# Kernel optimization log

Hardware: AMD Instinct MI355X
Metric: run time of the kernel (lower is better)

The kernel has to match this reference:

```python
import jax, jax.numpy as jnp
import numpy as np

D_MODEL = 512
NH_ATTN = 8
D_STATE = 64
HEADDIM = 128
D_INNER = 2 * D_MODEL          # 1024
NHEADS = D_INNER // HEADDIM    # 8
CONV_K = 4
CONV_DIM = D_INNER + 2 * D_STATE            # 1152
D_IN_PROJ = 2 * D_INNER + 2 * D_STATE + NHEADS  # 2184
B, S, M = 2, 2048, 1024
EPS = 1e-5


def setup_inputs() -> dict:
    key = jax.random.key(0)
    ks = jax.random.split(key, 10)
    s = 0.02
    return {
        'x': jax.random.normal(ks[0], (B, S, D_MODEL), dtype=jnp.float32),
        'memory': jax.random.normal(ks[1], (B, M, D_MODEL), dtype=jnp.float32),
        'pad_mask': jnp.ones((B, S, 1), dtype=jnp.float32),
        'ln1_g': jnp.ones((D_MODEL,)), 'ln1_b': jnp.zeros((D_MODEL,)),
        'ln2_g': jnp.ones((D_MODEL,)), 'ln2_b': jnp.zeros((D_MODEL,)),
        'W_in': jax.random.normal(ks[2], (D_IN_PROJ, D_MODEL)) * s,
        'conv_w': jax.random.normal(ks[3], (CONV_DIM, 1, CONV_K)) * s,
        'conv_b': jnp.zeros((CONV_DIM,)),
        'dt_bias': jnp.log(jnp.expm1(jax.random.uniform(ks[4], (NHEADS,), minval=0.001, maxval=0.1))),
        'A_log': jnp.log(jnp.arange(1, NHEADS + 1, dtype=jnp.float32)),
        'D_skip': jnp.ones((NHEADS,)),
        'rms_w': jnp.ones((D_INNER,)),
        'W_out': jax.random.normal(ks[5], (D_MODEL, D_INNER)) * s,
        'Wqkv': jax.random.normal(ks[6], (3 * D_MODEL, D_MODEL)) * s,
        'bqkv': jnp.zeros((3 * D_MODEL,)),
        'Wo': jax.random.normal(ks[7], (D_MODEL, D_MODEL)) * s,
        'bo': jnp.zeros((D_MODEL,)),
    }


def _layernorm(x, g, b):
    m = jnp.mean(x, axis=-1, keepdims=True)
    v = jnp.mean((x - m) ** 2, axis=-1, keepdims=True)
    return (x - m) * jax.lax.rsqrt(v + EPS) * g + b


def _mamba(x, W_in, conv_w, conv_b, dt_bias, A_log, D_skip, rms_w, W_out):
    b, s, _ = x.shape
    zxbcdt = x @ W_in.T                                     # [b,s,2184]
    z, xBC, dt = jnp.split(zxbcdt, [D_INNER, D_INNER + CONV_DIM], axis=-1)
    # causal depthwise conv over time on (x, B, C)
    xt = jnp.transpose(xBC, (0, 2, 1))                      # [b,C,s]
    xt = jax.lax.conv_general_dilated(
        xt, conv_w, (1,), [(CONV_K - 1, 0)],
        feature_group_count=CONV_DIM,
        dimension_numbers=('NCH', 'OIH', 'NCH'))
    xBC = jax.nn.silu(jnp.transpose(xt, (0, 2, 1)) + conv_b)
    xs, Bm, Cm = jnp.split(xBC, [D_INNER, D_INNER + D_STATE], axis=-1)
    dt = jax.nn.softplus(dt + dt_bias)                      # [b,s,H]
    A = -jnp.exp(A_log)                                     # [H]
    xh = xs.reshape(b, s, NHEADS, HEADDIM)                  # [b,s,H,P]

    def step(h, inps):
        dt_t, B_t, C_t, x_t = inps                          # [b,H],[b,N],[b,N],[b,H,P]
        decay = jnp.exp(dt_t * A)                           # [b,H]
        h = h * decay[..., None, None] + (dt_t[..., None, None] * x_t[..., None]) * B_t[:, None, None, :]
        y = jnp.einsum('bhpn,bn->bhp', h, C_t)
        return h, y

    h0 = jnp.zeros((b, NHEADS, HEADDIM, D_STATE), dtype=x.dtype)
    _, ys = jax.lax.scan(step, h0, (dt.transpose(1, 0, 2), Bm.transpose(1, 0, 2),
                                    Cm.transpose(1, 0, 2), xh.transpose(1, 0, 2, 3)))
    y = ys.transpose(1, 0, 2, 3) + D_skip[None, None, :, None] * xh
    y = y.reshape(b, s, D_INNER) * jax.nn.silu(z)           # gated
    y = y * jax.lax.rsqrt(jnp.mean(y * y, axis=-1, keepdims=True) + EPS) * rms_w
    return y @ W_out.T


def _cross_attn(q_in, memory, Wqkv, bqkv, Wo, bo):
    b, s, _ = q_in.shape
    m = memory.shape[1]
    dh = D_MODEL // NH_ATTN
    q = (q_in @ Wqkv[:D_MODEL].T + bqkv[:D_MODEL]).reshape(b, s, NH_ATTN, dh)
    k = (memory @ Wqkv[D_MODEL:2 * D_MODEL].T + bqkv[D_MODEL:2 * D_MODEL]).reshape(b, m, NH_ATTN, dh)
    v = (memory @ Wqkv[2 * D_MODEL:].T + bqkv[2 * D_MODEL:]).reshape(b, m, NH_ATTN, dh)
    scores = jnp.einsum('bqhd,bkhd->bhqk', q, k) / jnp.sqrt(jnp.asarray(dh, q.dtype))
    p = jax.nn.softmax(scores, axis=-1)
    out = jnp.einsum('bhqk,bkhd->bqhd', p, v).reshape(b, s, D_MODEL)
    return out @ Wo.T + bo


def reference(x, memory, pad_mask, ln1_g, ln1_b, ln2_g, ln2_b, W_in, conv_w, conv_b,
              dt_bias, A_log, D_skip, rms_w, W_out, Wqkv, bqkv, Wo, bo):
    residual = x
    xn = _layernorm(x, ln1_g, ln1_b) * pad_mask
    x = residual + _mamba(xn, W_in, conv_w, conv_b, dt_bias, A_log, D_skip, rms_w, W_out)
    h = _layernorm(x, ln2_g, ln2_b)
    x = x + _cross_attn(h, memory, Wqkv, bqkv, Wo, bo)
    return x
```

## Files before the change

### kernel.cpp

```cpp
#include <hip/hip_runtime.h>
#include <hip/hip_bf16.h>

typedef __hip_bfloat16 bf16;
typedef short v8s __attribute__((ext_vector_type(8)));
typedef short v4s __attribute__((ext_vector_type(4)));
typedef float v4f __attribute__((ext_vector_type(4)));

__device__ __forceinline__ void gll16(const bf16* g, bf16* l) {
    __builtin_amdgcn_global_load_lds(
        (const __attribute__((address_space(1))) unsigned int*)g,
        (__attribute__((address_space(3))) unsigned int*)l, 16, 0, 0);
}
__device__ __forceinline__ float bf2f(short s) {
    return __uint_as_float(((unsigned int)(unsigned short)s) << 16);
}

__global__ __launch_bounds__(256) void pre_kernel(
    const float* __restrict__ x, const float* __restrict__ g,
    const float* __restrict__ bt, const float* __restrict__ mask,
    bf16* __restrict__ xn,
    const float* __restrict__ W_in, const float* __restrict__ W_out,
    const float* __restrict__ Wqkv, const float* __restrict__ Wo,
    const float* __restrict__ mem,
    bf16* __restrict__ Winb, bf16* __restrict__ Woutb, bf16* __restrict__ Wqkvb,
    bf16* __restrict__ Wob, bf16* __restrict__ memb)
{
    int tid = threadIdx.x;
    if (blockIdx.x < 4096) {
        int row = blockIdx.x;
        const float* xr = x + (size_t)row * 512;
        float v0 = xr[tid], v1 = xr[tid + 256];
        float s = v0 + v1, ss = v0 * v0 + v1 * v1;
        #pragma unroll
        for (int o = 32; o; o >>= 1) { s += __shfl_xor(s, o); ss += __shfl_xor(ss, o); }
        __shared__ float l1[4], l2[4];
        if ((tid & 63) == 0) { l1[tid >> 6] = s; l2[tid >> 6] = ss; }
        __syncthreads();
        s = l1[0] + l1[1] + l1[2] + l1[3];
        ss = l2[0] + l2[1] + l2[2] + l2[3];
        float mean = s * (1.f / 512.f);
        float var = ss * (1.f / 512.f) - mean * mean;
        float rs = rsqrtf(var + 1e-5f);
        float mk = mask[row];
        xn[(size_t)row * 512 + tid] =
            __float2bfloat16(((v0 - mean) * rs * g[tid] + bt[tid]) * mk);
        xn[(size_t)row * 512 + tid + 256] =
            __float2bfloat16(((v1 - mean) * rs * g[tid + 256] + bt[tid + 256]) * mk);
        return;
    }
    int i = (blockIdx.x - 4096) * 256 + tid;
    const int E0 = 2184 * 512;
    const int E1 = E0 + 524288;
    const int E2 = E1 + 786432;
    const int E3 = E2 + 262144;
    const int E4 = E3 + 1048576;
    if (i < E0) {
        Winb[i] = __float2bfloat16(W_in[i]);
    } else if (i < E1) {
        int j = i - E0; Woutb[j] = __float2bfloat16(W_out[j]);
    } else if (i < E2) {
        int j = i - E1; Wqkvb[j] = __float2bfloat16(Wqkv[j]);
    } else if (i < E3) {
        int j = i - E2; Wob[j] = __float2bfloat16(Wo[j]);
    } else if (i < E4) {
        int j = i - E3; memb[j] = __float2bfloat16(mem[j]);
    }
}

__global__ __launch_bounds__(256) void ln_kernel(
    const float* __restrict__ x, const float* __restrict__ g,
    const float* __restrict__ bt, bf16* __restrict__ out)
{
    int row = blockIdx.x, tid = threadIdx.x;
    const float* xr = x + (size_t)row * 512;
    float v0 = xr[tid], v1 = xr[tid + 256];
    float s = v0 + v1, ss = v0 * v0 + v1 * v1;
    #pragma unroll
    for (int o = 32; o; o >>= 1) { s += __shfl_xor(s, o); ss += __shfl_xor(ss, o); }
    __shared__ float l1[4], l2[4];
    if ((tid & 63) == 0) { l1[tid >> 6] = s; l2[tid >> 6] = ss; }
    __syncthreads();
    s = l1[0] + l1[1] + l1[2] + l1[3];
    ss = l2[0] + l2[1] + l2[2] + l2[3];
    float mean = s * (1.f / 512.f);
    float var = ss * (1.f / 512.f) - mean * mean;
    float rs = rsqrtf(var + 1e-5f);
    out[(size_t)row * 512 + tid] =
        __float2bfloat16((v0 - mean) * rs * g[tid] + bt[tid]);
    out[(size_t)row * 512 + tid + 256] =
        __float2bfloat16((v1 - mean) * rs * g[tid + 256] + bt[tid + 256]);
}

__global__ __launch_bounds__(256) void gemm_bt(
    const bf16* __restrict__ Aall, const bf16* __restrict__ Wall,
    const float* __restrict__ bias, const float* __restrict__ resid,
    void* __restrict__ Cout,
    int M, int N, int K, int ldA, int ldW, int ldC,
    long sA1, long sA2, long sW1, long sW2, long sC1, long sC2,
    int zdiv, int outbf16)
{
    __shared__ bf16 lA[2][128 * 32];
    __shared__ bf16 lB[2][128 * 32];
    int z = blockIdx.z;
    int zb = z / zdiv, zh = z - zb * zdiv;
    const bf16* A = Aall + zb * sA1 + zh * sA2;
    const bf16* W = Wall + zb * sW1 + zh * sW2;
    long coff = zb * sC1 + zh * sC2;

    int bm = blockIdx.x * 128, bn = blockIdx.y * 128;
    int tid = threadIdx.x, lane = tid & 63, wv = tid >> 6;
    int wr = (wv >> 1) * 64, wc = (wv & 1) * 64;
    int lr15 = lane & 15, lk8 = (lane >> 4) * 8;

    v4f acc[4][4] = {};
    int sr = tid >> 2, sc = (tid & 3) * 8;
    const bf16* Abase = A + (size_t)(bm + sr) * ldA + sc;
    const bf16* Wbase = W + (size_t)(bn + sr) * ldW + sc;

    int nt = K >> 5, cur = 0;
    gll16(Abase, &lA[0][tid * 8]);
    gll16(Abase + (size_t)64 * ldA, &lA[0][tid * 8 + 2048]);
    gll16(Wbase, &lB[0][tid * 8]);
    gll16(Wbase + (size_t)64 * ldW, &lB[0][tid * 8 + 2048]);
    __syncthreads();
    for (int t = 0; t < nt; ++t) {
        if (t + 1 < nt) {
            int k0 = (t + 1) * 32;
            gll16(Abase + k0, &lA[cur ^ 1][tid * 8]);
            gll16(Abase + (size_t)64 * ldA + k0, &lA[cur ^ 1][tid * 8 + 2048]);
            gll16(Wbase + k0, &lB[cur ^ 1][tid * 8]);
            gll16(Wbase + (size_t)64 * ldW + k0, &lB[cur ^ 1][tid * 8 + 2048]);
        }
        v8s af[4], bfr[4];
        #pragma unroll
        for (int i = 0; i < 4; ++i)
            af[i] = *(const v8s*)&lA[cur][(wr + i * 16 + lr15) * 32 + lk8];
        #pragma unroll
        for (int i = 0; i < 4; ++i)
            bfr[i] = *(const v8s*)&lB[cur][(wc + i * 16 + lr15) * 32 + lk8];
        #pragma unroll
        for (int mi = 0; mi < 4; ++mi)
            #pragma unroll
            for (int ni = 0; ni < 4; ++ni)
                acc[mi][ni] = __builtin_amdgcn_mfma_f32_16x16x32_bf16(
                    af[mi], bfr[ni], acc[mi][ni], 0, 0, 0);
        __syncthreads();
        cur ^= 1;
    }
    int r0 = bm + wr + (lane >> 4) * 4;
    int c0 = bn + wc + lr15;
    #pragma unroll
    for (int mi = 0; mi < 4; ++mi) {
        #pragma unroll
        for (int ni = 0; ni < 4; ++ni) {
            int col = c0 + ni * 16;
            if (col < N) {
                float bv = bias ? bias[col] : 0.f;
                #pragma unroll
                for (int r = 0; r < 4; ++r) {
                    int row = r0 + mi * 16 + r;
                    long idx = coff + (long)row * ldC + col;
                    float v = acc[mi][ni][r] + bv;
                    if (resid) v += resid[idx];
                    if (outbf16) ((bf16*)Cout)[idx] = __float2bfloat16(v);
                    else ((float*)Cout)[idx] = v;
                }
            }
        }
    }
}

__global__ __launch_bounds__(256) void gemm64(
    const bf16* __restrict__ Aall, const bf16* __restrict__ Wall,
    const float* __restrict__ bias, const float* __restrict__ resid,
    void* __restrict__ Cout,
    int M, int N, int K, int ldA, int ldW, int ldC,
    long sA1, long sA2, long sW1, long sW2, long sC1, long sC2,
    int zdiv, int outbf16)
{
    __shared__ bf16 lA[2][64 * 32];
    __shared__ bf16 lB[2][64 * 32];
    int z = blockIdx.z;
    int zb = z / zdiv, zh = z - zb * zdiv;
    const bf16* A = Aall + zb * sA1 + zh * sA2;
    const bf16* W = Wall + zb * sW1 + zh * sW2;
    long coff = zb * sC1 + zh * sC2;

    int bm = blockIdx.x * 64, bn = blockIdx.y * 64;
    int tid = threadIdx.x, lane = tid & 63, wv = tid >> 6;
    int wr = (wv >> 1) * 32, wc = (wv & 1) * 32;
    int lr15 = lane & 15, lk8 = (lane >> 4) * 8;

    v4f acc[2][2] = {};
    int sr = tid >> 2, sc = (tid & 3) * 8;
    const bf16* Abase = A + (size_t)(bm + sr) * ldA + sc;
    const bf16* Wbase = W + (size_t)(bn + sr) * ldW + sc;

    int nt = K >> 5, cur = 0;
    gll16(Abase, &lA[0][tid * 8]);
    gll16(Wbase, &lB[0][tid * 8]);
    __syncthreads();
    for (int t = 0; t < nt; ++t) {
        if (t + 1 < nt) {
            int k0 = (t + 1) * 32;
            gll16(Abase + k0, &lA[cur ^ 1][tid * 8]);
            gll16(Wbase + k0, &lB[cur ^ 1][tid * 8]);
        }
        v8s a0 = *(const v8s*)&lA[cur][(wr + lr15) * 32 + lk8];
        v8s a1 = *(const v8s*)&lA[cur][(wr + 16 + lr15) * 32 + lk8];
        v8s b0 = *(const v8s*)&lB[cur][(wc + lr15) * 32 + lk8];
        v8s b1 = *(const v8s*)&lB[cur][(wc + 16 + lr15) * 32 + lk8];
        acc[0][0] = __builtin_amdgcn_mfma_f32_16x16x32_bf16(a0, b0, acc[0][0], 0, 0, 0);
        acc[0][1] = __builtin_amdgcn_mfma_f32_16x16x32_bf16(a0, b1, acc[0][1], 0, 0, 0);
        acc[1][0] = __builtin_amdgcn_mfma_f32_16x16x32_bf16(a1, b0, acc[1][0], 0, 0, 0);
        acc[1][1] = __builtin_amdgcn_mfma_f32_16x16x32_bf16(a1, b1, acc[1][1], 0, 0, 0);
        __syncthreads();
        cur ^= 1;
    }
    int r0 = bm + wr + (lane >> 4) * 4;
    int c0 = bn + wc + lr15;
    #pragma unroll
    for (int mi = 0; mi < 2; ++mi) {
        #pragma unroll
        for (int ni = 0; ni < 2; ++ni) {
            int col = c0 + ni * 16;
            if (col < N) {
                float bv = bias ? bias[col] : 0.f;
                #pragma unroll
                for (int r = 0; r < 4; ++r) {
                    int row = r0 + mi * 16 + r;
                    long idx = coff + (long)row * ldC + col;
                    float v = acc[mi][ni][r] + bv;
                    if (resid) v += resid[idx];
                    if (outbf16) ((bf16*)Cout)[idx] = __float2bfloat16(v);
                    else ((float*)Cout)[idx] = v;
                }
            }
        }
    }
}

__global__ __launch_bounds__(256) void flash_attn(
    const bf16* __restrict__ qb, const bf16* __restrict__ kvb,
    const bf16* __restrict__ vT, bf16* __restrict__ attn)
{
    __shared__ bf16 lK[2][128 * 64];
    __shared__ bf16 lV[2][64 * 128];
    __shared__ bf16 lP[4][16 * 128];
    int z = blockIdx.z;
    int b = z >> 3, h = z & 7;
    int q0 = blockIdx.x * 64;
    int tid = threadIdx.x, lane = tid & 63, wv = tid >> 6;
    int l15 = lane & 15, l4 = lane >> 4, l7 = lane & 7;

    const bf16* Qg = qb + (size_t)(b * 2048 + q0) * 512 + h * 64;
    const bf16* Kg = kvb + (size_t)b * 1024 * 1024 + h * 64;
    const bf16* Vg = vT + (size_t)z * 64 * 1024;

    v8s af[2];
    #pragma unroll
    for (int ks = 0; ks < 2; ++ks)
        af[ks] = *(const v8s*)(Qg + (size_t)(wv * 16 + l15) * 512 + (ks * 4 + l4) * 8);

    #pragma unroll
    for (int pass = 0; pass < 4; ++pass) {
        int s = pass * 256 + tid;
        int kr = s >> 3, kc = s & 7;
        gll16(Kg + (size_t)kr * 1024 + ((kc ^ (kr & 7)) << 3), &lK[0][s * 8]);
        int vr = s >> 4, vc = s & 15;
        int vsw = (vc & 8) | ((vc & 7) ^ (vr & 7));
        gll16(Vg + (size_t)vr * 1024 + (vsw << 3), &lV[0][s * 8]);
    }
    __syncthreads();

    v4f o[4] = {};
    v4f m_run = (v4f){-1e30f, -1e30f, -1e30f, -1e30f};
    v4f l_run = (v4f){0.f, 0.f, 0.f, 0.f};
    bf16* lPw = &lP[wv][0];

    int cur = 0;
    #pragma unroll 1
    for (int t = 0; t < 8; ++t) {
        if (t + 1 < 8) {
            int k0n = (t + 1) * 128;
            #pragma unroll
            for (int pass = 0; pass < 4; ++pass) {
                int s = pass * 256 + tid;
                int kr = s >> 3, kc = s & 7;
                gll16(Kg + (size_t)(k0n + kr) * 1024 + ((kc ^ (kr & 7)) << 3),
                      &lK[cur ^ 1][s * 8]);
                int vr = s >> 4, vc = s & 15;
                int vsw = (vc & 8) | ((vc & 7) ^ (vr & 7));
                gll16(Vg + (size_t)vr * 1024 + k0n + (vsw << 3), &lV[cur ^ 1][s * 8]);
            }
        }
        v4f s_acc[8];
        #pragma unroll
        for (int kn = 0; kn < 8; ++kn) {
            s_acc[kn] = (v4f){0.f, 0.f, 0.f, 0.f};
            #pragma unroll
            for (int ks = 0; ks < 2; ++ks) {
                v8s kv = *(const v8s*)&lK[cur][(kn * 16 + l15) * 64 +
                                               (((ks * 4 + l4) ^ l7) << 3)];
                s_acc[kn] = __builtin_amdgcn_mfma_f32_16x16x32_bf16(
                    af[ks], kv, s_acc[kn], 0, 0, 0);
            }
        }
        v4f tm;
        #pragma unroll
        for (int r = 0; r < 4; ++r) {
            float m0 = fmaxf(fmaxf(s_acc[0][r], s_acc[1][r]),
                             fmaxf(s_acc[2][r], s_acc[3][r]));
            float m1 = fmaxf(fmaxf(s_acc[4][r], s_acc[5][r]),
                             fmaxf(s_acc[6][r], s_acc[7][r]));
            tm[r] = fmaxf(m0, m1);
        }
        #pragma unroll
        for (int off = 8; off >= 1; off >>= 1)
            #pragma unroll
            for (int r = 0; r < 4; ++r)
                tm[r] = fmaxf(tm[r], __shfl_xor(tm[r], off));
        v4f mnew, alpha;
        #pragma unroll
        for (int r = 0; r < 4; ++r) {
            mnew[r] = fmaxf(m_run[r], 0.125f * tm[r]);
            alpha[r] = __expf(m_run[r] - mnew[r]);
        }
        m_run = mnew;
        v4f rs = {0.f, 0.f, 0.f, 0.f};
        #pragma unroll
        for (int kn = 0; kn < 8; ++kn)
            #pragma unroll
            for (int r = 0; r < 4; ++r) {
                float pv = __expf(0.125f * s_acc[kn][r] - mnew[r]);
                s_acc[kn][r] = pv;
                rs[r] += pv;
            }
        #pragma unroll
        for (int off = 8; off >= 1; off >>= 1)
            #pragma unroll
            for (int r = 0; r < 4; ++r)
                rs[r] += __shfl_xor(rs[r], off);
        #pragma unroll
        for (int r = 0; r < 4; ++r)
            l_run[r] = l_run[r] * alpha[r] + rs[r];
        #pragma unroll
        for (int ni = 0; ni < 4; ++ni)
            #pragma unroll
            for (int r = 0; r < 4; ++r)
                o[ni][r] *= alpha[r];
        #pragma unroll
        for (int kn = 0; kn < 8; ++kn)
            #pragma unroll
            for (int r = 0; r < 4; ++r) {
                int row = l4 * 4 + r;
                int col = kn * 16 + l15;
                int c = col >> 3;
                int csw = (c & 8) | ((c & 7) ^ (row & 7));
                lPw[row * 128 + (csw << 3) + (col & 7)] =
                    __float2bfloat16(s_acc[kn][r]);
            }
        #pragma unroll
        for (int ni = 0; ni < 4; ++ni)
            #pragma unroll
            for (int ks = 0; ks < 4; ++ks) {
                int ck = ks * 4 + l4;
                int psw = (ck & 8) | ((ck & 7) ^ l7);
                v8s pv = *(const v8s*)&lPw[l15 * 128 + (psw << 3)];
                v8s vv = *(const v8s*)&lV[cur][(ni * 16 + l15) * 128 + (psw << 3)];
                o[ni] = __builtin_amdgcn_mfma_f32_16x16x32_bf16(
                    pv, vv, o[ni], 0, 0, 0);
            }
        __syncthreads();
        cur ^= 1;
    }
    v4f inv;
    #pragma unroll
    for (int r = 0; r < 4; ++r) inv[r] = 1.f / l_run[r];
    #pragma unroll
    for (int ni = 0; ni < 4; ++ni)
        #pragma unroll
        for (int r = 0; r < 4; ++r) {
            int row = q0 + wv * 16 + l4 * 4 + r;
            int col = h * 64 + ni * 16 + l15;
            attn[(size_t)(b * 2048 + row) * 512 + col] =
                __float2bfloat16(o[ni][r] * inv[r]);
        }
}

__global__ __launch_bounds__(256) void conv_dt(
    const bf16* __restrict__ zx, const float* __restrict__ cw,
    const float* __restrict__ cb, bf16* __restrict__ out,
    const float* __restrict__ dt_bias, const float* __restrict__ A_log,
    float* __restrict__ dtb, float* __restrict__ decb)
{
    int tid = threadIdx.x;
    if (blockIdx.x >= 576) {
        int i = (blockIdx.x - 576) * 256 + tid;
        if (i >= 32768) return;
        int h = i & 7, row = i >> 3;
        float d = bf2f(((const short*)zx)[(size_t)row * 2184 + 2176 + h]) + dt_bias[h];
        float sp = d > 20.f ? d : log1pf(expf(d));
        dtb[i] = sp;
        decb[i] = expf(-expf(A_log[h]) * sp);
        return;
    }
    int idx = blockIdx.x * 256 + tid;
    int c4 = (idx % 288) * 4;
    int tb = (idx / 288) % 256;
    int b  = idx / (288 * 256);
    int t0 = tb * 8;
    const bf16* base = zx + (size_t)b * 2048 * 2184 + 1024 + c4;
    bf16* ob = out + ((size_t)(b * 2048 + t0)) * 1152 + c4;

    float wt[4][4];
    #pragma unroll
    for (int k = 0; k < 4; ++k)
        #pragma unroll
        for (int j = 0; j < 4; ++j) wt[j][k] = cw[(c4 + k) * 4 + j];
    v4f bias = *(const v4f*)(cb + c4);

    v4f r[11];
    #pragma unroll
    for (int j = 0; j < 11; ++j) {
        int ts = t0 - 3 + j;
        if (ts >= 0) {
            v4s raw = *(const v4s*)(base + (size_t)ts * 2184);
            #pragma unroll
            for (int k = 0; k < 4; ++k) r[j][k] = bf2f(raw[k]);
        } else r[j] = (v4f){0.f, 0.f, 0.f, 0.f};
    }
    #pragma unroll
    for (int t = 0; t < 8; ++t) {
        v4f acc = bias;
        #pragma unroll
        for (int k = 0; k < 4; ++k)
            acc[k] += wt[0][k] * r[t][k] + wt[1][k] * r[t + 1][k]
                    + wt[2][k] * r[t + 2][k] + wt[3][k] * r[t + 3][k];
        v4s res;
        #pragma unroll
        for (int k = 0; k < 4; ++k) {
            float v = acc[k] / (1.f + expf(-acc[k]));
            res[k] = (short)__bfloat16_as_ushort(__float2bfloat16(v));
        }
        *(v4s*)(ob + (size_t)t * 1152) = res;
    }
}

__global__ __launch_bounds__(256) void scan_p1(
    const bf16* __restrict__ conv, const float* __restrict__ dtb,
    const float* __restrict__ decb, const float* __restrict__ A_log,
    bf16* __restrict__ slocal, float* __restrict__ cdec)
{
    int chunk = blockIdx.x, bh = blockIdx.y;
    int b = bh >> 3, h = bh & 7;
    int tid = threadIdx.x;
    int wv = tid >> 6, lane = tid & 63;
    int nh = lane >> 5, psub = lane & 31;
    int p = wv * 32 + psub;
    __shared__ float lx[32][128];
    __shared__ float lB[32][64];
    __shared__ float ldt[32], ldec[32];
    const bf16* cb_ = conv + (size_t)b * 2048 * 1152;
    int t0 = chunk * 32;
    #pragma unroll
    for (int pass = 0; pass < 2; ++pass) {
        int s = pass * 256 + tid;
        int row = s >> 4, c8 = (s & 15) * 8;
        v8s raw = *(const v8s*)(cb_ + (size_t)(t0 + row) * 1152 + h * 128 + c8);
        v4f lo, hi;
        #pragma unroll
        for (int j = 0; j < 4; ++j) { lo[j] = bf2f(raw[j]); hi[j] = bf2f(raw[j + 4]); }
        *(v4f*)&lx[row][c8] = lo;
        *(v4f*)&lx[row][c8 + 4] = hi;
    }
    {
        int s = tid;
        int row = s >> 3, c8 = (s & 7) * 8;
        v8s raw = *(const v8s*)(cb_ + (size_t)(t0 + row) * 1152 + 1024 + c8);
        v4f lo, hi;
        #pragma unroll
        for (int j = 0; j < 4; ++j) { lo[j] = bf2f(raw[j]); hi[j] = bf2f(raw[j + 4]); }
        *(v4f*)&lB[row][c8] = lo;
        *(v4f*)&lB[row][c8 + 4] = hi;
    }
    if (tid < 32) {
        int ri = (b * 2048 + t0 + tid) * 8 + h;
        ldt[tid] = dtb[ri]; ldec[tid] = decb[ri];
    }
    __syncthreads();
    v4f hs[8] = {};
    float sdt = 0.f;
    #pragma unroll 2
    for (int t = 0; t < 32; ++t) {
        float dtv = ldt[t], dec = ldec[t];
        float c1 = dtv * lx[t][p];
        const v4f* Bp = (const v4f*)&lB[t][nh * 32];
        #pragma unroll
        for (int i = 0; i < 8; ++i) hs[i] = hs[i] * dec + Bp[i] * c1;
        sdt += dtv;
    }
    if (tid == 0) cdec[bh * 64 + chunk] = expf(-expf(A_log[h]) * sdt);
    bf16* S = slocal + ((size_t)bh * 64 + chunk) * 8192;
    #pragma unroll
    for (int i = 0; i < 8; ++i)
        #pragma unroll
        for (int j = 0; j < 4; ++j)
            S[(nh * 32 + i * 4 + j) * 128 + p] = __float2bfloat16(hs[i][j]);
}

__global__ __launch_bounds__(256) void scan_comb(
    const bf16* __restrict__ slocal, const float* __restrict__ cdec,
    bf16* __restrict__ hinit)
{
    int e = blockIdx.x * 256 + threadIdx.x;
    int bh = e >> 13, np = e & 8191;
    size_t base = (size_t)bh * 524288 + np;
    const float* cd = cdec + bh * 64;
    float hi = 0.f;
    for (int c = 0; c < 64; ++c) {
        size_t idx = base + (size_t)c * 8192;
        hinit[idx] = __float2bfloat16(hi);
        hi = hi * cd[c] + __bfloat162float(slocal[idx]);
    }
}

__global__ __launch_bounds__(256) void scan_p3(
    const bf16* __restrict__ conv, const float* __restrict__ dtb,
    const float* __restrict__ decb, const bf16* __restrict__ hinit,
    const float* __restrict__ Dskip, bf16* __restrict__ ybuf)
{
    int chunk = blockIdx.x, bh = blockIdx.y;
    int b = bh >> 3, h = bh & 7;
    int tid = threadIdx.x;
    int wv = tid >> 6, lane = tid & 63;
    int nh = lane >> 5, psub = lane & 31;
    int p = wv * 32 + psub;
    __shared__ float lx[32][128];
    __shared__ float lB[32][64];
    __shared__ float lC[32][64];
    __shared__ float ldt[32], ldec[32];
    const bf16* cb_ = conv + (size_t)b * 2048 * 1152;
    int t0 = chunk * 32;
    #pragma unroll
    for (int pass = 0; pass < 2; ++pass) {
        int s = pass * 256 + tid;
        int row = s >> 4, c8 = (s & 15) * 8;
        v8s raw = *(const v8s*)(cb_ + (size_t)(t0 + row) * 1152 + h * 128 + c8);
        v4f lo, hi;
        #pragma unroll
        for (int j = 0; j < 4; ++j) { lo[j] = bf2f(raw[j]); hi[j] = bf2f(raw[j + 4]); }
        *(v4f*)&lx[row][c8] = lo;
        *(v4f*)&lx[row][c8 + 4] = hi;
    }
    {
        int s = tid;
        int row = s >> 3, c8 = (s & 7) * 8;
        v8s rawB = *(const v8s*)(cb_ + (size_t)(t0 + row) * 1152 + 1024 + c8);
        v8s rawC = *(const v8s*)(cb_ + (size_t)(t0 + row) * 1152 + 1088 + c8);
        v4f lo, hi;
        #pragma unroll
        for (int j = 0; j < 4; ++j) { lo[j] = bf2f(rawB[j]); hi[j] = bf2f(rawB[j + 4]); }
        *(v4f*)&lB[row][c8] = lo;
        *(v4f*)&lB[row][c8 + 4] = hi;
        #pragma unroll
        for (int j = 0; j < 4; ++j) { lo[j] = bf2f(rawC[j]); hi[j] = bf2f(rawC[j + 4]); }
        *(v4f*)&lC[row][c8] = lo;
        *(v4f*)&lC[row][c8 + 4] = hi;
    }
    if (tid < 32) {
        int ri = (b * 2048 + t0 + tid) * 8 + h;
        ldt[tid] = dtb[ri]; ldec[tid] = decb[ri];
    }
    __syncthreads();
    v4f hs[8];
    const bf16* H = hinit + ((size_t)bh * 64 + chunk) * 8192;
    #pragma unroll
    for (int i = 0; i < 8; ++i)
        #pragma unroll
        for (int j = 0; j < 4; ++j)
            hs[i][j] = __bfloat162float(H[(nh * 32 + i * 4 + j) * 128 + p]);
    float Dk = Dskip[h];
    #pragma unroll 2
    for (int t = 0; t < 32; ++t) {
        float dtv = ldt[t], dec = ldec[t];
        float xv = lx[t][p];
        float c1 = dtv * xv;
        const v4f* Bp = (const v4f*)&lB[t][nh * 32];
        const v4f* Cp = (const v4f*)&lC[t][nh * 32];
        v4f ya = {0.f, 0.f, 0.f, 0.f};
        #pragma unroll
        for (int i = 0; i < 8; ++i) {
            hs[i] = hs[i] * dec + Bp[i] * c1;
            ya += hs[i] * Cp[i];
        }
        float part = ya[0] + ya[1] + ya[2] + ya[3];
        part += __shfl_xor(part, 32);
        if (nh == 0)
            ybuf[((size_t)(b * 2048 + t0 + t)) * 1024 + h * 128 + p] =
                __float2bfloat16(part + Dk * xv);
    }
}

__global__ __launch_bounds__(256) void gate_rms(
    const bf16* __restrict__ ybuf, const bf16* __restrict__ zx,
    const float* __restrict__ rms_w, bf16* __restrict__ out)
{
    int row = blockIdx.x, tid = threadIdx.x;
    int i0 = tid * 4;
    v4s yv = *(const v4s*)(ybuf + (size_t)row * 1024 + i0);
    v4s zv = *(const v4s*)(zx + (size_t)row * 2184 + i0);
    v4f rw = *(const v4f*)(rms_w + i0);
    float vals[4];
    float ss = 0.f;
    #pragma unroll
    for (int j = 0; j < 4; ++j) {
        float y = bf2f(yv[j]);
        float z = bf2f(zv[j]);
        float g = y * (z / (1.f + expf(-z)));
        vals[j] = g;
        ss += g * g;
    }
    #pragma unroll
    for (int o = 32; o; o >>= 1) ss += __shfl_xor(ss, o);
    __shared__ float l[4];
    if ((tid & 63) == 0) l[tid >> 6] = ss;
    __syncthreads();
    ss = l[0] + l[1] + l[2] + l[3];
    float rs = rsqrtf(ss * (1.f / 1024.f) + 1e-5f);
    v4s o4;
    #pragma unroll
    for (int j = 0; j < 4; ++j)
        o4[j] = (short)__bfloat16_as_ushort(__float2bfloat16(vals[j] * rs * rw[j]));
    *(v4s*)(out + (size_t)row * 1024 + i0) = o4;
}

__global__ __launch_bounds__(256) void v_transpose(const bf16* __restrict__ kvb,
                                                   bf16* __restrict__ vT) {
    __shared__ bf16 t[64][68];
    int bh = blockIdx.y, b = bh >> 3, h = bh & 7;
    int m0 = blockIdx.x * 64;
    int tid = threadIdx.x;
    #pragma unroll
    for (int pass = 0; pass < 2; ++pass) {
        int s = pass * 256 + tid;
        int row = s >> 3, c8 = (s & 7) * 8;
        v8s v = *(const v8s*)(kvb + ((size_t)(b * 1024 + m0 + row)) * 1024 + 512 +
                              h * 64 + c8);
        *(v8s*)&t[row][c8] = v;
    }
    __syncthreads();
    #pragma unroll
    for (int pass = 0; pass < 2; ++pass) {
        int s = pass * 256 + tid;
        int d = s >> 3, m8 = (s & 7) * 8;
        bf16 tmp[8];
        #pragma unroll
        for (int j = 0; j < 8; ++j) tmp[j] = t[m8 + j][d];
        *(v8s*)(vT + ((size_t)(bh * 64 + d)) * 1024 + m0 + m8) = *(v8s*)&tmp[0];
    }
}

extern "C" void kernel_launch(void* const* d_in, const int* in_sizes, int n_in,
                              void* d_out, int out_size, void* d_ws, size_t ws_size,
                              hipStream_t stream) {
    (void)in_sizes; (void)n_in; (void)out_size; (void)ws_size;
    const float* x       = (const float*)d_in[0];
    const float* memory  = (const float*)d_in[1];
    const float* mask    = (const float*)d_in[2];
    const float* ln1_g   = (const float*)d_in[3];
    const float* ln1_b   = (const float*)d_in[4];
    const float* ln2_g   = (const float*)d_in[5];
    const float* ln2_b   = (const float*)d_in[6];
    const float* W_in    = (const float*)d_in[7];
    const float* conv_w  = (const float*)d_in[8];
    const float* conv_b  = (const float*)d_in[9];
    const float* dt_bias = (const float*)d_in[10];
    const float* A_log   = (const float*)d_in[11];
    const float* D_skip  = (const float*)d_in[12];
    const float* rms_w   = (const float*)d_in[13];
    const float* W_out   = (const float*)d_in[14];
    const float* Wqkv    = (const float*)d_in[15];
    const float* bqkv    = (const float*)d_in[16];
    const float* Wo      = (const float*)d_in[17];
    const float* bo      = (const float*)d_in[18];
    float* out = (float*)d_out;

    char* w = (char*)d_ws;
    bf16*  xn     = (bf16*)(w + 0);
    bf16*  Winb   = (bf16*)(w + 4194304);
    bf16*  Woutb  = (bf16*)(w + 6430720);
    bf16*  Wqkvb  = (bf16*)(w + 7479296);
    bf16*  Wob    = (bf16*)(w + 9052160);
    bf16*  memb   = (bf16*)(w + 9576448);
    bf16*  zx     = (bf16*)(w + 11673600);
    bf16*  conv   = (bf16*)(w + 47456256);
    float* dtb    = (float*)(w + 66330624);
    float* decb   = (float*)(w + 66461696);
    bf16*  ybuf   = (bf16*)(w + 66592768);
    bf16*  slocal = (bf16*)(w + 83369984);
    bf16*  hinit  = (bf16*)(w + 100147200);
    bf16*  ybf    = (bf16*)(w + 83369984);
    float* x2     = (float*)(w + 100147200);
    bf16*  hb     = (bf16*)(w + 108535808);
    bf16*  qb     = (bf16*)(w + 112730112);
    float* cdec   = (float*)(w + 116924416);
    bf16*  kvb    = (bf16*)(w + 116928512);
    bf16*  vT     = (bf16*)(w + 121122816);
    bf16*  attn   = (bf16*)(w + 123219968);
    bf16*  gout   = (bf16*)(w + 75497472);
    gout = (bf16*)(w + 29564928);
    (void)ybf;

    pre_kernel<<<18704, 256, 0, stream>>>(x, ln1_g, ln1_b, mask, xn,
                                          W_in, W_out, Wqkv, Wo, memory,
                                          Winb, Woutb, Wqkvb, Wob, memb);

    gemm_bt<<<dim3(32, 18, 1), 256, 0, stream>>>(
        xn, Winb, nullptr, nullptr, (void*)zx,
        4096, 2184, 512, 512, 512, 2184,
        0, 0, 0, 0, 0, 0, 1, 1);

    conv_dt<<<704, 256, 0, stream>>>(zx, conv_w, conv_b, conv,
                                     dt_bias, A_log, dtb, decb);

    scan_p1<<<dim3(64, 16), 256, 0, stream>>>(conv, dtb, decb, A_log, slocal, cdec);
    scan_comb<<<512, 256, 0, stream>>>(slocal, cdec, hinit);
    scan_p3<<<dim3(64, 16), 256, 0, stream>>>(conv, dtb, decb, hinit, D_skip, ybuf);

    gate_rms<<<4096, 256, 0, stream>>>(ybuf, zx, rms_w, gout);

    gemm64<<<dim3(64, 8, 1), 256, 0, stream>>>(
        gout, Woutb, nullptr, x, (void*)x2,
        4096, 512, 1024, 1024, 1024, 512,
        0, 0, 0, 0, 0, 0, 1, 0);

    ln_kernel<<<4096, 256, 0, stream>>>(x2, ln2_g, ln2_b, hb);

    gemm64<<<dim3(64, 8, 1), 256, 0, stream>>>(
        hb, Wqkvb, bqkv, nullptr, (void*)qb,
        4096, 512, 512, 512, 512, 512, 0, 0, 0, 0, 0, 0, 1, 1);
    gemm64<<<dim3(32, 16, 1), 256, 0, stream>>>(
        memb, Wqkvb + 512 * 512, bqkv + 512, nullptr, (void*)kvb,
        2048, 1024, 512, 512, 512, 1024, 0, 0, 0, 0, 0, 0, 1, 1);

    v_transpose<<<dim3(16, 16), 256, 0, stream>>>(kvb, vT);

    flash_attn<<<dim3(32, 1, 16), 256, 0, stream>>>(qb, kvb, vT, attn);

    gemm64<<<dim3(64, 8, 1), 256, 0, stream>>>(
        attn, Wob, bo, x2, (void*)out,
        4096, 512, 512, 512, 512, 512,
        0, 0, 0, 0, 0, 0, 1, 0);
}
```

Baseline: 196.3 us.

## Fuse causal conv and dt softplus into scan kernels; fuse V transpose into KV GEMM

Removes the standalone conv_dt kernel. Both scan_p1 and scan_p3 now load raw zx rows, with a 3-row halo, into LDS and compute the depthwise conv, SiLU, softplus(dt) and the decay inline. This drops the intermediate conv/dt/decay buffers and one launch, at the cost of computing the conv twice, once in each scan pass. The V transpose kernel is also removed: the KV projection GEMM epilogue now writes the transposed V directly as packed 4-element stores.

```diff
diff --git a/kernel.cpp b/kernel.cpp
--- a/kernel.cpp
+++ b/kernel.cpp
@@ -13,6 +13,9 @@
 }
 __device__ __forceinline__ float bf2f(short s) {
     return __uint_as_float(((unsigned int)(unsigned short)s) << 16);
+}
+__device__ __forceinline__ short f2bfs(float f) {
+    return (short)__bfloat16_as_ushort(__float2bfloat16(f));
 }
 
 __global__ __launch_bounds__(256) void pre_kernel(
@@ -176,7 +179,7 @@
     void* __restrict__ Cout,
     int M, int N, int K, int ldA, int ldW, int ldC,
     long sA1, long sA2, long sW1, long sW2, long sC1, long sC2,
-    int zdiv, int outbf16)
+    int zdiv, int outbf16, bf16* __restrict__ vTout)
 {
     __shared__ bf16 lA[2][64 * 32];
     __shared__ bf16 lB[2][64 * 32];
@@ -226,14 +229,26 @@
             int col = c0 + ni * 16;
             if (col < N) {
                 float bv = bias ? bias[col] : 0.f;
+                float vals[4];
                 #pragma unroll
                 for (int r = 0; r < 4; ++r) {
                     int row = r0 + mi * 16 + r;
                     long idx = coff + (long)row * ldC + col;
                     float v = acc[mi][ni][r] + bv;
                     if (resid) v += resid[idx];
+                    vals[r] = v;
                     if (outbf16) ((bf16*)Cout)[idx] = __float2bfloat16(v);
                     else ((float*)Cout)[idx] = v;
+                }
+                if (vTout && col >= 512) {
+                    int d = col - 512;
+                    int row0 = r0 + mi * 16;
+                    int bb = row0 >> 10, m0 = row0 & 1023;
+                    v4s pk;
+                    #pragma unroll
+                    for (int r = 0; r < 4; ++r) pk[r] = f2bfs(vals[r]);
+                    *(v4s*)(vTout + (((size_t)(bb * 8 + (d >> 6)) * 64 + (d & 63))
+                                     * 1024 + m0)) = pk;
                 }
             }
         }
@@ -388,68 +403,10 @@
         }
 }
 
-__global__ __launch_bounds__(256) void conv_dt(
+__global__ __launch_bounds__(256) void scan_p1(
     const bf16* __restrict__ zx, const float* __restrict__ cw,
-    const float* __restrict__ cb, bf16* __restrict__ out,
-    const float* __restrict__ dt_bias, const float* __restrict__ A_log,
-    float* __restrict__ dtb, float* __restrict__ decb)
-{
-    int tid = threadIdx.x;
-    if (blockIdx.x >= 576) {
-        int i = (blockIdx.x - 576) * 256 + tid;
-        if (i >= 32768) return;
-        int h = i & 7, row = i >> 3;
-        float d = bf2f(((const short*)zx)[(size_t)row * 2184 + 2176 + h]) + dt_bias[h];
-        float sp = d > 20.f ? d : log1pf(expf(d));
-        dtb[i] = sp;
-        decb[i] = expf(-expf(A_log[h]) * sp);
-        return;
-    }
-    int idx = blockIdx.x * 256 + tid;
-    int c4 = (idx % 288) * 4;
-    int tb = (idx / 288) % 256;
-    int b  = idx / (288 * 256);
-    int t0 = tb * 8;
-    const bf16* base = zx + (size_t)b * 2048 * 2184 + 1024 + c4;
-    bf16* ob = out + ((size_t)(b * 2048 + t0)) * 1152 + c4;
-
-    float wt[4][4];
-    #pragma unroll
-    for (int k = 0; k < 4; ++k)
-        #pragma unroll
-        for (int j = 0; j < 4; ++j) wt[j][k] = cw[(c4 + k) * 4 + j];
-    v4f bias = *(const v4f*)(cb + c4);
-
-    v4f r[11];
-    #pragma unroll
-    for (int j = 0; j < 11; ++j) {
-        int ts = t0 - 3 + j;
-        if (ts >= 0) {
-            v4s raw = *(const v4s*)(base + (size_t)ts * 2184);
-            #pragma unroll
-            for (int k = 0; k < 4; ++k) r[j][k] = bf2f(raw[k]);
-        } else r[j] = (v4f){0.f, 0.f, 0.f, 0.f};
-    }
-    #pragma unroll
-    for (int t = 0; t < 8; ++t) {
-        v4f acc = bias;
-        #pragma unroll
-        for (int k = 0; k < 4; ++k)
-            acc[k] += wt[0][k] * r[t][k] + wt[1][k] * r[t + 1][k]
-                    + wt[2][k] * r[t + 2][k] + wt[3][k] * r[t + 3][k];
-        v4s res;
-        #pragma unroll
-        for (int k = 0; k < 4; ++k) {
-            float v = acc[k] / (1.f + expf(-acc[k]));
-            res[k] = (short)__bfloat16_as_ushort(__float2bfloat16(v));
-        }
-        *(v4s*)(ob + (size_t)t * 1152) = res;
-    }
-}
-
-__global__ __launch_bounds__(256) void scan_p1(
-    const bf16* __restrict__ conv, const float* __restrict__ dtb,
-    const float* __restrict__ decb, const float* __restrict__ A_log,
+    const float* __restrict__ cb, const float* __restrict__ dt_bias,
+    const float* __restrict__ A_log,
     bf16* __restrict__ slocal, float* __restrict__ cdec)
 {
     int chunk = blockIdx.x, bh = blockIdx.y;
@@ -458,35 +415,84 @@
     int wv = tid >> 6, lane = tid & 63;
     int nh = lane >> 5, psub = lane & 31;
     int p = wv * 32 + psub;
-    __shared__ float lx[32][128];
+    __shared__ bf16 rawx[35][136];
+    __shared__ bf16 rawB[35][72];
+    __shared__ bf16 lxb[32][128];
     __shared__ float lB[32][64];
+    __shared__ v4f lwx[128];
+    __shared__ v4f lwB[64];
+    __shared__ float lcb[192];
     __shared__ float ldt[32], ldec[32];
-    const bf16* cb_ = conv + (size_t)b * 2048 * 1152;
+    const bf16* zb_ = zx + (size_t)b * 2048 * 2184;
     int t0 = chunk * 32;
-    #pragma unroll
-    for (int pass = 0; pass < 2; ++pass) {
-        int s = pass * 256 + tid;
-        int row = s >> 4, c8 = (s & 15) * 8;
-        v8s raw = *(const v8s*)(cb_ + (size_t)(t0 + row) * 1152 + h * 128 + c8);
-        v4f lo, hi;
-        #pragma unroll
-        for (int j = 0; j < 4; ++j) { lo[j] = bf2f(raw[j]); hi[j] = bf2f(raw[j + 4]); }
-        *(v4f*)&lx[row][c8] = lo;
-        *(v4f*)&lx[row][c8 + 4] = hi;
-    }
+    for (int s = tid; s < 560; s += 256) {
+        int rr = s >> 4, c8 = (s & 15) * 8;
+        int zr = t0 - 3 + rr;
+        v8s v = {};
+        if (zr >= 0) v = *(const v8s*)(zb_ + (size_t)zr * 2184 + 1024 + h * 128 + c8);
+        *(v8s*)&rawx[rr][c8] = v;
+    }
+    for (int s = tid; s < 280; s += 256) {
+        int rr = s >> 3, c8 = (s & 7) * 8;
+        int zr = t0 - 3 + rr;
+        v8s v = {};
+        if (zr >= 0) v = *(const v8s*)(zb_ + (size_t)zr * 2184 + 2048 + c8);
+        *(v8s*)&rawB[rr][c8] = v;
+    }
+    if (tid < 128) {
+        lwx[tid] = *(const v4f*)(cw + (h * 128 + tid) * 4);
+        lcb[tid] = cb[h * 128 + tid];
+    } else if (tid < 192) {
+        int c = tid - 128;
+        lwB[c] = *(const v4f*)(cw + (1024 + c) * 4);
+        lcb[128 + c] = cb[1024 + c];
+    } else if (tid < 224) {
+        int t = tid - 192;
+        float d = bf2f(((const short*)zb_)[(size_t)(t0 + t) * 2184 + 2176 + h])
+                  + dt_bias[h];
+        float sp = d > 20.f ? d : log1pf(expf(d));
+        ldt[t] = sp;
+        ldec[t] = expf(-expf(A_log[h]) * sp);
+    }
+    __syncthreads();
     {
-        int s = tid;
-        int row = s >> 3, c8 = (s & 7) * 8;
-        v8s raw = *(const v8s*)(cb_ + (size_t)(t0 + row) * 1152 + 1024 + c8);
-        v4f lo, hi;
-        #pragma unroll
-        for (int j = 0; j < 4; ++j) { lo[j] = bf2f(raw[j]); hi[j] = bf2f(raw[j + 4]); }
-        *(v4f*)&lB[row][c8] = lo;
-        *(v4f*)&lB[row][c8 + 4] = hi;
-    }
-    if (tid < 32) {
-        int ri = (b * 2048 + t0 + tid) * 8 + h;
-        ldt[tid] = dtb[ri]; ldec[tid] = decb[ri];
+        int t = tid >> 3;
+        int pc = (tid & 7) * 16;
+        #pragma unroll
+        for (int half = 0; half < 2; ++half) {
+            int pcc = pc + half * 8;
+            float acc[8];
+            #pragma unroll
+            for (int k = 0; k < 8; ++k) acc[k] = lcb[pcc + k];
+            #pragma unroll
+            for (int j = 0; j < 4; ++j) {
+                v8s rv = *(const v8s*)&rawx[t + j][pcc];
+                #pragma unroll
+                for (int k = 0; k < 8; ++k)
+                    acc[k] += lwx[pcc + k][j] * bf2f(rv[k]);
+            }
+            v8s ov;
+            #pragma unroll
+            for (int k = 0; k < 8; ++k) {
+                float v = acc[k] / (1.f + __expf(-acc[k]));
+                ov[k] = f2bfs(v);
+            }
+            *(v8s*)&lxb[t][pcc] = ov;
+        }
+        int bc = (tid & 7) * 8;
+        float accB[8];
+        #pragma unroll
+        for (int k = 0; k < 8; ++k) accB[k] = lcb[128 + bc + k];
+        #pragma unroll
+        for (int j = 0; j < 4; ++j) {
+            v8s rv = *(const v8s*)&rawB[t + j][bc];
+            #pragma unroll
+            for (int k = 0; k < 8; ++k)
+                accB[k] += lwB[bc + k][j] * bf2f(rv[k]);
+        }
+        #pragma unroll
+        for (int k = 0; k < 8; ++k)
+            lB[t][bc + k] = accB[k] / (1.f + __expf(-accB[k]));
     }
     __syncthreads();
     v4f hs[8] = {};
@@ -494,7 +500,7 @@
     #pragma unroll 2
     for (int t = 0; t < 32; ++t) {
         float dtv = ldt[t], dec = ldec[t];
-        float c1 = dtv * lx[t][p];
+        float c1 = dtv * bf2f(*(const short*)&lxb[t][p]);
         const v4f* Bp = (const v4f*)&lB[t][nh * 32];
         #pragma unroll
         for (int i = 0; i < 8; ++i) hs[i] = hs[i] * dec + Bp[i] * c1;
@@ -526,8 +532,9 @@
 }
 
 __global__ __launch_bounds__(256) void scan_p3(
-    const bf16* __restrict__ conv, const float* __restrict__ dtb,
-    const float* __restrict__ decb, const bf16* __restrict__ hinit,
+    const bf16* __restrict__ zx, const float* __restrict__ cw,
+    const float* __restrict__ cb, const float* __restrict__ dt_bias,
+    const float* __restrict__ A_log, const bf16* __restrict__ hinit,
     const float* __restrict__ Dskip, bf16* __restrict__ ybuf)
 {
     int chunk = blockIdx.x, bh = blockIdx.y;
@@ -536,41 +543,93 @@
     int wv = tid >> 6, lane = tid & 63;
     int nh = lane >> 5, psub = lane & 31;
     int p = wv * 32 + psub;
-    __shared__ float lx[32][128];
+    __shared__ bf16 rawx[35][136];
+    __shared__ bf16 rawBC[35][136];
+    __shared__ bf16 lxb[32][128];
     __shared__ float lB[32][64];
     __shared__ float lC[32][64];
+    __shared__ v4f lwx[128];
+    __shared__ v4f lwBC[128];
+    __shared__ float lcb[256];
     __shared__ float ldt[32], ldec[32];
-    const bf16* cb_ = conv + (size_t)b * 2048 * 1152;
+    const bf16* zb_ = zx + (size_t)b * 2048 * 2184;
     int t0 = chunk * 32;
-    #pragma unroll
-    for (int pass = 0; pass < 2; ++pass) {
-        int s = pass * 256 + tid;
-        int row = s >> 4, c8 = (s & 15) * 8;
-        v8s raw = *(const v8s*)(cb_ + (size_t)(t0 + row) * 1152 + h * 128 + c8);
-        v4f lo, hi;
-        #pragma unroll
-        for (int j = 0; j < 4; ++j) { lo[j] = bf2f(raw[j]); hi[j] = bf2f(raw[j + 4]); }
-        *(v4f*)&lx[row][c8] = lo;
-        *(v4f*)&lx[row][c8 + 4] = hi;
+    for (int s = tid; s < 560; s += 256) {
+        int rr = s >> 4, c8 = (s & 15) * 8;
+        int zr = t0 - 3 + rr;
+        v8s v = {};
+        if (zr >= 0) v = *(const v8s*)(zb_ + (size_t)zr * 2184 + 1024 + h * 128 + c8);
+        *(v8s*)&rawx[rr][c8] = v;
+        v8s v2 = {};
+        if (zr >= 0) v2 = *(const v8s*)(zb_ + (size_t)zr * 2184 + 2048 + c8);
+        *(v8s*)&rawBC[rr][c8] = v2;
+    }
+    if (tid < 128) {
+        lwx[tid] = *(const v4f*)(cw + (h * 128 + tid) * 4);
+        lcb[tid] = cb[h * 128 + tid];
+    } else if (tid < 224) {
+        int c = tid - 128;
+        lwBC[c] = *(const v4f*)(cw + (1024 + c) * 4);
+        lcb[128 + c] = cb[1024 + c];
+    }
+    if (tid >= 224) {
+        int c = tid - 224 + 96;
+        lwBC[c] = *(const v4f*)(cw + (1024 + c) * 4);
+        lcb[128 + c] = cb[1024 + c];
+    }
+    __syncthreads();
+    if (tid < 32) {
+        float d = bf2f(((const short*)zb_)[(size_t)(t0 + tid) * 2184 + 2176 + h])
+                  + dt_bias[h];
+        float sp = d > 20.f ? d : log1pf(expf(d));
+        ldt[tid] = sp;
+        ldec[tid] = expf(-expf(A_log[h]) * sp);
     }
     {
-        int s = tid;
-        int row = s >> 3, c8 = (s & 7) * 8;
-        v8s rawB = *(const v8s*)(cb_ + (size_t)(t0 + row) * 1152 + 1024 + c8);
-        v8s rawC = *(const v8s*)(cb_ + (size_t)(t0 + row) * 1152 + 1088 + c8);
-        v4f lo, hi;
-        #pragma unroll
-        for (int j = 0; j < 4; ++j) { lo[j] = bf2f(rawB[j]); hi[j] = bf2f(rawB[j + 4]); }
-        *(v4f*)&lB[row][c8] = lo;
-        *(v4f*)&lB[row][c8 + 4] = hi;
-        #pragma unroll
-        for (int j = 0; j < 4; ++j) { lo[j] = bf2f(rawC[j]); hi[j] = bf2f(rawC[j + 4]); }
-        *(v4f*)&lC[row][c8] = lo;
-        *(v4f*)&lC[row][c8 + 4] = hi;
-    }
-    if (tid < 32) {
-        int ri = (b * 2048 + t0 + tid) * 8 + h;
-        ldt[tid] = dtb[ri]; ldec[tid] = decb[ri];
+        int t = tid >> 3;
+        int pc = (tid & 7) * 16;
+        #pragma unroll
+        for (int half = 0; half < 2; ++half) {
+            int pcc = pc + half * 8;
+            float acc[8];
+            #pragma unroll
+            for (int k = 0; k < 8; ++k) acc[k] = lcb[pcc + k];
+            #pragma unroll
+            for (int j = 0; j < 4; ++j) {
+                v8s rv = *(const v8s*)&rawx[t + j][pcc];
+                #pragma unroll
+                for (int k = 0; k < 8; ++k)
+                    acc[k] += lwx[pcc + k][j] * bf2f(rv[k]);
+            }
+            v8s ov;
+            #pragma unroll
+            for (int k = 0; k < 8; ++k) {
+                float v = acc[k] / (1.f + __expf(-acc[k]));
+                ov[k] = f2bfs(v);
+            }
+            *(v8s*)&lxb[t][pcc] = ov;
+        }
+        #pragma unroll
+        for (int half = 0; half < 2; ++half) {
+            int cc = (tid & 7) * 16 + half * 8;
+            float acc[8];
+            #pragma unroll
+            for (int k = 0; k < 8; ++k) acc[k] = lcb[128 + cc + k];
+            #pragma unroll
+            for (int j = 0; j < 4; ++j) {
+                v8s rv = *(const v8s*)&rawBC[t + j][cc];
+                #pragma unroll
+                for (int k = 0; k < 8; ++k)
+                    acc[k] += lwBC[cc + k][j] * bf2f(rv[k]);
+            }
+            #pragma unroll
+            for (int k = 0; k < 8; ++k) {
+                float v = acc[k] / (1.f + __expf(-acc[k]));
+                int ch = cc + k;
+                if (ch < 64) lB[t][ch] = v;
+                else lC[t][ch - 64] = v;
+            }
+        }
     }
     __syncthreads();
     v4f hs[8];
@@ -584,7 +643,7 @@
     #pragma unroll 2
     for (int t = 0; t < 32; ++t) {
         float dtv = ldt[t], dec = ldec[t];
-        float xv = lx[t][p];
+        float xv = bf2f(*(const short*)&lxb[t][p]);
         float c1 = dtv * xv;
         const v4f* Bp = (const v4f*)&lB[t][nh * 32];
         const v4f* Cp = (const v4f*)&lC[t][nh * 32];
@@ -631,34 +690,8 @@
     v4s o4;
     #pragma unroll
     for (int j = 0; j < 4; ++j)
-        o4[j] = (short)__bfloat16_as_ushort(__float2bfloat16(vals[j] * rs * rw[j]));
+        o4[j] = f2bfs(vals[j] * rs * rw[j]);
     *(v4s*)(out + (size_t)row * 1024 + i0) = o4;
-}
-
-__global__ __launch_bounds__(256) void v_transpose(const bf16* __restrict__ kvb,
-                                                   bf16* __restrict__ vT) {
-    __shared__ bf16 t[64][68];
-    int bh = blockIdx.y, b = bh >> 3, h = bh & 7;
-    int m0 = blockIdx.x * 64;
-    int tid = threadIdx.x;
-    #pragma unroll
-    for (int pass = 0; pass < 2; ++pass) {
-        int s = pass * 256 + tid;
-        int row = s >> 3, c8 = (s & 7) * 8;
-        v8s v = *(const v8s*)(kvb + ((size_t)(b * 1024 + m0 + row)) * 1024 + 512 +
-                              h * 64 + c8);
-        *(v8s*)&t[row][c8] = v;
-    }
-    __syncthreads();
-    #pragma unroll
-    for (int pass = 0; pass < 2; ++pass) {
-        int s = pass * 256 + tid;
-        int d = s >> 3, m8 = (s & 7) * 8;
-        bf16 tmp[8];
-        #pragma unroll
-        for (int j = 0; j < 8; ++j) tmp[j] = t[m8 + j][d];
-        *(v8s*)(vT + ((size_t)(bh * 64 + d)) * 1024 + m0 + m8) = *(v8s*)&tmp[0];
-    }
 }
 
 extern "C" void kernel_launch(void* const* d_in, const int* in_sizes, int n_in,
@@ -694,13 +727,10 @@
     bf16*  Wob    = (bf16*)(w + 9052160);
     bf16*  memb   = (bf16*)(w + 9576448);
     bf16*  zx     = (bf16*)(w + 11673600);
-    bf16*  conv   = (bf16*)(w + 47456256);
-    float* dtb    = (float*)(w + 66330624);
-    float* decb   = (float*)(w + 66461696);
+    bf16*  gout   = (bf16*)(w + 29564928);
     bf16*  ybuf   = (bf16*)(w + 66592768);
     bf16*  slocal = (bf16*)(w + 83369984);
     bf16*  hinit  = (bf16*)(w + 100147200);
-    bf16*  ybf    = (bf16*)(w + 83369984);
     float* x2     = (float*)(w + 100147200);
     bf16*  hb     = (bf16*)(w + 108535808);
     bf16*  qb     = (bf16*)(w + 112730112);
@@ -708,9 +738,6 @@
     bf16*  kvb    = (bf16*)(w + 116928512);
     bf16*  vT     = (bf16*)(w + 121122816);
     bf16*  attn   = (bf16*)(w + 123219968);
-    bf16*  gout   = (bf16*)(w + 75497472);
-    gout = (bf16*)(w + 29564928);
-    (void)ybf;
 
     pre_kernel<<<18704, 256, 0, stream>>>(x, ln1_g, ln1_b, mask, xn,
                                           W_in, W_out, Wqkv, Wo, memory,
@@ -721,35 +748,32 @@
         4096, 2184, 512, 512, 512, 2184,
         0, 0, 0, 0, 0, 0, 1, 1);
 
-    conv_dt<<<704, 256, 0, stream>>>(zx, conv_w, conv_b, conv,
-                                     dt_bias, A_log, dtb, decb);
-
-    scan_p1<<<dim3(64, 16), 256, 0, stream>>>(conv, dtb, decb, A_log, slocal, cdec);
+    scan_p1<<<dim3(64, 16), 256, 0, stream>>>(zx, conv_w, conv_b, dt_bias, A_log,
+                                              slocal, cdec);
     scan_comb<<<512, 256, 0, stream>>>(slocal, cdec, hinit);
-    scan_p3<<<dim3(64, 16), 256, 0, stream>>>(conv, dtb, decb, hinit, D_skip, ybuf);
+    scan_p3<<<dim3(64, 16), 256, 0, stream>>>(zx, conv_w, conv_b, dt_bias, A_log,
+                                              hinit, D_skip, ybuf);
 
     gate_rms<<<4096, 256, 0, stream>>>(ybuf, zx, rms_w, gout);
 
     gemm64<<<dim3(64, 8, 1), 256, 0, stream>>>(
         gout, Woutb, nullptr, x, (void*)x2,
         4096, 512, 1024, 1024, 1024, 512,
-        0, 0, 0, 0, 0, 0, 1, 0);
+        0, 0, 0, 0, 0, 0, 1, 0, nullptr);
 
     ln_kernel<<<4096, 256, 0, stream>>>(x2, ln2_g, ln2_b, hb);
 
     gemm64<<<dim3(64, 8, 1), 256, 0, stream>>>(
         hb, Wqkvb, bqkv, nullptr, (void*)qb,
-        4096, 512, 512, 512, 512, 512, 0, 0, 0, 0, 0, 0, 1, 1);
+        4096, 512, 512, 512, 512, 512, 0, 0, 0, 0, 0, 0, 1, 1, nullptr);
     gemm64<<<dim3(32, 16, 1), 256, 0, stream>>>(
         memb, Wqkvb + 512 * 512, bqkv + 512, nullptr, (void*)kvb,
-        2048, 1024, 512, 512, 512, 1024, 0, 0, 0, 0, 0, 0, 1, 1);
-
-    v_transpose<<<dim3(16, 16), 256, 0, stream>>>(kvb, vT);
+        2048, 1024, 512, 512, 512, 1024, 0, 0, 0, 0, 0, 0, 1, 1, vT);
 
     flash_attn<<<dim3(32, 1, 16), 256, 0, stream>>>(qb, kvb, vT, attn);
 
     gemm64<<<dim3(64, 8, 1), 256, 0, stream>>>(
         attn, Wob, bo, x2, (void*)out,
         4096, 512, 512, 512, 512, 512,
-        0, 0, 0, 0, 0, 0, 1, 0);
-}
+        0, 0, 0, 0, 0, 0, 1, 0, nullptr);
+}
```

New measurement: 205.8 us. 4.8% more time.
